# Optimization experiments

Hardware: AMD Instinct MI355X
Metric: run time of the kernel (lower is better)

The kernel has to match this reference:

```python
import jax, jax.numpy as jnp
import numpy as np
from jax import lax

RSM_K = 35
PFM_K = 31


def _box_sum(x, k):
    # Separable zero-padded box sum, equivalent to conv2d with a uniform kxk
    # kernel and padding=k//2 (odd k -> SAME). x: [B,1,H,W]
    p = k // 2
    pad = ((0, 0), (0, 0), (p, p), (0, 0))
    x = lax.reduce_window(x, 0.0, lax.add, (1, 1, k, 1), (1, 1, 1, 1), pad)
    pad = ((0, 0), (0, 0), (0, 0), (p, p))
    x = lax.reduce_window(x, 0.0, lax.add, (1, 1, 1, k), (1, 1, 1, 1), pad)
    return x


def _dilate(x, k):
    # Separable morphological dilation == max_pool2d(kernel=k, stride=1, pad=k//2).
    # -inf padding matches torch's max_pool2d padding semantics for 0/1 masks.
    p = k // 2
    ninf = -jnp.inf
    pad = ((0, 0), (0, 0), (p, p), (0, 0))
    x = lax.reduce_window(x, ninf, lax.max, (1, 1, k, 1), (1, 1, 1, 1), pad)
    pad = ((0, 0), (0, 0), (0, 0), (p, p))
    x = lax.reduce_window(x, ninf, lax.max, (1, 1, 1, k), (1, 1, 1, 1), pad)
    return x


def setup_inputs() -> dict:
    key = jax.random.key(0)
    # Sparse binary lesion mask, values exactly 0.0 / 1.0, shape [B,1,H,W]
    masks = (jax.random.uniform(key, (32, 1, 768, 768)) < 0.02).astype(jnp.float32)
    return {"masks": masks}


def reference(masks):
    # RSM: probability map = uniform 35x35 box average (conv2d with 1/k^2 kernel)
    rsm = _box_sum(masks, RSM_K) * (1.0 / (RSM_K * RSM_K))  # [B,1,H,W]
    # PFM: 1 = lesion, 0 = surrounding (inside 31x31 dilation), 2 = ignore
    dilated = _dilate(masks, PFM_K)
    pfm = jnp.where(masks > 0.5, 1, jnp.where(dilated > 0.5, 0, 2))
    pfm = pfm.astype(jnp.int32)[:, 0, :, :]  # [B,H,W]
    return rsm, pfm
```

## Files before the change

### kernel.cpp

```cpp
#include <hip/hip_runtime.h>


#define BATCH 32
#define HH 768
#define WW 768
#define NPIX (HH * WW)

constexpr int TYO  = 48;
constexpr int HALO = 17;
constexpr int ROWS = TYO + 2 * HALO;
constexpr int NSEG = 12;
constexpr int SSEG = NSEG + 2;
constexpr int NT   = 768;
constexpr int NG   = 4;
constexpr int RPG  = TYO / NG;
constexpr int CT   = 192;

__global__ __launch_bounds__(NT)
void label_gen_fused(const float* __restrict__ in, float* __restrict__ out) {
    __shared__ unsigned long long sbits[ROWS][SSEG];
    __shared__ unsigned int hm[ROWS][CT];

    const int tid  = threadIdx.x;
    const int lane = tid & 63;
    const int wv   = tid >> 6;
    const int y0   = blockIdx.x * TYO;
    const int b    = blockIdx.y;
    const float* __restrict__ src = in + (size_t)b * NPIX;

    for (int lr = wv; lr < ROWS; lr += NT / 64) {
        const int r = y0 - HALO + lr;
        unsigned long long bb[NSEG];
        if ((unsigned)r < (unsigned)HH) {
            const float* rp = src + (size_t)r * WW;
            #pragma unroll
            for (int j = 0; j < NSEG; ++j)
                bb[j] = __ballot(rp[64 * j + lane] > 0.5f);
        } else {
            #pragma unroll
            for (int j = 0; j < NSEG; ++j) bb[j] = 0ull;
        }
        if (lane == 0) {
            sbits[lr][0] = 0ull;
            #pragma unroll
            for (int j = 0; j < NSEG; ++j) sbits[lr][j + 1] = bb[j];
            sbits[lr][SSEG - 1] = 0ull;
        }
    }
    __syncthreads();

    {
        const int r0 = tid / CT;
        const int ct = tid - r0 * CT;
        const int c0 = 4 * ct;
        const int s  = c0 - HALO;
        const int q  = (s >> 6) + 1;
        const int sh = s & 63;
        const unsigned long long M35 = (1ull << 35) - 1;
        for (int lr = r0; lr < ROWS; lr += NG) {
            const unsigned long long w =
                (sbits[lr][q] >> sh) | (sbits[lr][q + 1] << (64 - sh));
            const int h0 = (int)__popcll(w & M35);
            const int h1 = h0 + (int)((w >> 35) & 1) - (int)(w & 1);
            const int h2 = h1 + (int)((w >> 36) & 1) - (int)((w >> 1) & 1);
            const int h3 = h2 + (int)((w >> 37) & 1) - (int)((w >> 2) & 1);
            unsigned long long sm = w | (w >> 1);
            sm |= sm >> 2; sm |= sm >> 4; sm |= sm >> 8;
            const unsigned int o4 = (unsigned int)(((sm >> 2) | (sm >> 17)) & 0xFull);
            const unsigned int m4 = (unsigned int)((w >> 17) & 0xFull);
            const unsigned int mb =
                (((m4 & 1u) | ((m4 & 2u) << 7) | ((m4 & 4u) << 14) | ((m4 & 8u) << 21)) << 6);
            const unsigned int ob =
                (((o4 & 1u) | ((o4 & 2u) << 7) | ((o4 & 4u) << 14) | ((o4 & 8u) << 21)) << 7);
            hm[lr][ct] = (unsigned)h0 | ((unsigned)h1 << 8) | ((unsigned)h2 << 16)
                       | ((unsigned)h3 << 24) | mb | ob;
        }
    }
    __syncthreads();

    const int g   = tid / CT;
    const int ct  = tid - g * CT;
    const int c0  = 4 * ct;
    const int yb  = y0 + RPG * g;
    const int lr0 = RPG * g;

    const unsigned int M6 = 0x003F003Fu;
    const unsigned int M1 = 0x01010101u;

    unsigned int vA = 0, vB = 0;
    unsigned int c31 = 0;
    unsigned int ring_e[2], ring_l[2];
    #pragma unroll
    for (int k = 0; k < 35; ++k) {
        const unsigned int x = hm[lr0 + k][ct];
        vA += x & M6;
        vB += (x >> 8) & M6;
        if (k >= 2 && k <= 32) c31 += (x >> 7) & M1;
        if (k == 0)  ring_l[0] = x;
        if (k == 1)  ring_l[1] = x;
        if (k == 33) ring_e[0] = x;
        if (k == 34) ring_e[1] = x;
    }

    float* orow = out + (size_t)b * NPIX + (size_t)yb * WW + c0;
    float* prow = orow + (size_t)BATCH * NPIX;

    for (int i = 0; i < RPG; ++i) {
        const int lr = lr0 + HALO + i;
        const unsigned int xc = hm[lr][ct];

        float4 r4, p4;
        r4.x = (float)(vA & 0xFFFFu) * (1.0f / 1225.0f);
        r4.y = (float)(vB & 0xFFFFu) * (1.0f / 1225.0f);
        r4.z = (float)(vA >> 16)     * (1.0f / 1225.0f);
        r4.w = (float)(vB >> 16)     * (1.0f / 1225.0f);
        p4.x = ((xc >> 6) & 1u)  ? 1.0f : ((c31 & 0xFFu)         ? 0.0f : 2.0f);
        p4.y = ((xc >> 14) & 1u) ? 1.0f : (((c31 >> 8) & 0xFFu)  ? 0.0f : 2.0f);
        p4.z = ((xc >> 22) & 1u) ? 1.0f : (((c31 >> 16) & 0xFFu) ? 0.0f : 2.0f);
        p4.w = ((xc >> 30) & 1u) ? 1.0f : ((c31 >> 24)           ? 0.0f : 2.0f);

        *(float4*)orow = r4;
        *(float4*)prow = p4;
        orow += WW; prow += WW;

        if (i < RPG - 1) {
            const unsigned int xe   = hm[lr + 18][ct];
            const unsigned int xl31 = hm[lr0 + 2 + i][ct];
            const unsigned int xe31 = ring_e[i & 1];
            const unsigned int xl   = ring_l[i & 1];
            ring_e[i & 1] = xe;
            ring_l[i & 1] = xl31;
            vA  = (vA + (xe & M6)) - (xl & M6);
            vB  = (vB + ((xe >> 8) & M6)) - ((xl >> 8) & M6);
            c31 = (c31 + ((xe31 >> 7) & M1)) - ((xl31 >> 7) & M1);
        }
    }
}

extern "C" void kernel_launch(void* const* d_in, const int* in_sizes, int n_in,
                              void* d_out, int out_size, void* d_ws, size_t ws_size,
                              hipStream_t stream) {
    const float* masks = (const float*)d_in[0];
    float* out = (float*)d_out;
    dim3 grid(HH / TYO, BATCH);
    label_gen_fused<<<grid, NT, 0, stream>>>(masks, out);
}
```

Before: 211.8 us.

## Split fused kernel into horizontal-map and vertical-slide kernels via workspace

Splits the single fused kernel into two launches. The first computes the packed per-row horizontal box counts and mask/dilation bits once per row and writes them to a global workspace. The second reads that workspace and does the vertical sliding-window sums and output writes. This removes the recomputation of the halo rows (34 extra rows per 48-row tile) and the shared-memory footprint, at the cost of a second launch and a workspace round-trip of NPIX/4 words per image. The original fused kernel is kept as a fallback when the workspace is too small.

```diff
diff --git a/kernel.cpp b/kernel.cpp
--- a/kernel.cpp
+++ b/kernel.cpp
@@ -6,108 +6,99 @@
 #define WW 768
 #define NPIX (HH * WW)
 
-constexpr int TYO  = 48;
-constexpr int HALO = 17;
-constexpr int ROWS = TYO + 2 * HALO;
-constexpr int NSEG = 12;
-constexpr int SSEG = NSEG + 2;
-constexpr int NT   = 768;
-constexpr int NG   = 4;
-constexpr int RPG  = TYO / NG;
-constexpr int CT   = 192;
-
-__global__ __launch_bounds__(NT)
-void label_gen_fused(const float* __restrict__ in, float* __restrict__ out) {
-    __shared__ unsigned long long sbits[ROWS][SSEG];
-    __shared__ unsigned int hm[ROWS][CT];
-
-    const int tid  = threadIdx.x;
-    const int lane = tid & 63;
-    const int wv   = tid >> 6;
-    const int y0   = blockIdx.x * TYO;
+constexpr int K1_RPB = 16;
+
+__global__ __launch_bounds__(256)
+void hmap_kernel(const float* __restrict__ in, unsigned int* __restrict__ hmg) {
+    __shared__ unsigned long long sb[4][14];
+    const int lane = threadIdx.x & 63;
+    const int wv   = threadIdx.x >> 6;
     const int b    = blockIdx.y;
+    const int r0   = blockIdx.x * K1_RPB;
     const float* __restrict__ src = in + (size_t)b * NPIX;
-
-    for (int lr = wv; lr < ROWS; lr += NT / 64) {
-        const int r = y0 - HALO + lr;
-        unsigned long long bb[NSEG];
-        if ((unsigned)r < (unsigned)HH) {
-            const float* rp = src + (size_t)r * WW;
-            #pragma unroll
-            for (int j = 0; j < NSEG; ++j)
-                bb[j] = __ballot(rp[64 * j + lane] > 0.5f);
-        } else {
-            #pragma unroll
-            for (int j = 0; j < NSEG; ++j) bb[j] = 0ull;
-        }
+    unsigned int* __restrict__ dst = hmg + (size_t)b * (NPIX / 4);
+    const unsigned long long M35 = (1ull << 35) - 1;
+    auto bit = [](unsigned long long w, int k) -> unsigned {
+        return (unsigned)((w >> k) & 1ull);
+    };
+
+    for (int r = r0 + wv; r < r0 + K1_RPB; r += 4) {
+        const float* rp = src + (size_t)r * WW;
+        unsigned long long bb[12];
+        #pragma unroll
+        for (int j = 0; j < 12; ++j) bb[j] = __ballot(rp[64 * j + lane] > 0.5f);
         if (lane == 0) {
-            sbits[lr][0] = 0ull;
-            #pragma unroll
-            for (int j = 0; j < NSEG; ++j) sbits[lr][j + 1] = bb[j];
-            sbits[lr][SSEG - 1] = 0ull;
-        }
-    }
-    __syncthreads();
-
-    {
-        const int r0 = tid / CT;
-        const int ct = tid - r0 * CT;
-        const int c0 = 4 * ct;
-        const int s  = c0 - HALO;
-        const int q  = (s >> 6) + 1;
-        const int sh = s & 63;
-        const unsigned long long M35 = (1ull << 35) - 1;
-        for (int lr = r0; lr < ROWS; lr += NG) {
+            sb[wv][0] = 0ull;
+            #pragma unroll
+            for (int j = 0; j < 12; ++j) sb[wv][j + 1] = bb[j];
+            sb[wv][13] = 0ull;
+        }
+        __builtin_amdgcn_wave_barrier();
+        #pragma unroll
+        for (int it = 0; it < 3; ++it) {
+            const int gi = it * 64 + lane;
+            const int s  = 4 * gi - 17;
+            const int q  = (s >> 6) + 1;
+            const int sh = s & 63;
             const unsigned long long w =
-                (sbits[lr][q] >> sh) | (sbits[lr][q + 1] << (64 - sh));
-            const int h0 = (int)__popcll(w & M35);
-            const int h1 = h0 + (int)((w >> 35) & 1) - (int)(w & 1);
-            const int h2 = h1 + (int)((w >> 36) & 1) - (int)((w >> 1) & 1);
-            const int h3 = h2 + (int)((w >> 37) & 1) - (int)((w >> 2) & 1);
+                (sb[wv][q] >> sh) | (sb[wv][q + 1] << (64 - sh));
+            const unsigned h0 = (unsigned)__popcll(w & M35);
+            const unsigned h1 = h0 + bit(w, 35) - bit(w, 0);
+            const unsigned h2 = h1 + bit(w, 36) - bit(w, 1);
+            const unsigned h3 = h2 + bit(w, 37) - bit(w, 2);
             unsigned long long sm = w | (w >> 1);
             sm |= sm >> 2; sm |= sm >> 4; sm |= sm >> 8;
-            const unsigned int o4 = (unsigned int)(((sm >> 2) | (sm >> 17)) & 0xFull);
-            const unsigned int m4 = (unsigned int)((w >> 17) & 0xFull);
-            const unsigned int mb =
-                (((m4 & 1u) | ((m4 & 2u) << 7) | ((m4 & 4u) << 14) | ((m4 & 8u) << 21)) << 6);
-            const unsigned int ob =
-                (((o4 & 1u) | ((o4 & 2u) << 7) | ((o4 & 4u) << 14) | ((o4 & 8u) << 21)) << 7);
-            hm[lr][ct] = (unsigned)h0 | ((unsigned)h1 << 8) | ((unsigned)h2 << 16)
-                       | ((unsigned)h3 << 24) | mb | ob;
-        }
-    }
-    __syncthreads();
-
-    const int g   = tid / CT;
-    const int ct  = tid - g * CT;
-    const int c0  = 4 * ct;
+            const unsigned o4 = (unsigned)(((sm >> 2) | (sm >> 17)) & 0xFull);
+            const unsigned m4 = (unsigned)((w >> 17) & 0xFull);
+            const unsigned x = h0 | (h1 << 8) | (h2 << 16) | (h3 << 24)
+                             | ((m4 & 1u) << 6)  | ((m4 & 2u) << 13)
+                             | ((m4 & 4u) << 20) | ((m4 & 8u) << 27)
+                             | ((o4 & 1u) << 7)  | ((o4 & 2u) << 14)
+                             | ((o4 & 4u) << 21) | ((o4 & 8u) << 28);
+            dst[(size_t)r * 192 + gi] = x;
+        }
+        __builtin_amdgcn_wave_barrier();
+    }
+}
+
+constexpr int TYO = 48;
+constexpr int RPG = 12;
+
+__global__ __launch_bounds__(768)
+void vslide_kernel(const unsigned int* __restrict__ hmg, float* __restrict__ out) {
+    const int tid = threadIdx.x;
+    const int g   = tid / 192;
+    const int ct  = tid - g * 192;
+    const int y0  = blockIdx.x * TYO;
+    const int b   = blockIdx.y;
     const int yb  = y0 + RPG * g;
-    const int lr0 = RPG * g;
-
-    const unsigned int M6 = 0x003F003Fu;
-    const unsigned int M1 = 0x01010101u;
-
-    unsigned int vA = 0, vB = 0;
-    unsigned int c31 = 0;
-    unsigned int ring_e[2], ring_l[2];
+    const unsigned int* __restrict__ hb = hmg + (size_t)b * (NPIX / 4) + ct;
+    auto ld = [&](int r) -> unsigned {
+        return ((unsigned)r < (unsigned)HH) ? hb[(size_t)r * 192] : 0u;
+    };
+    const unsigned M6 = 0x003F003Fu;
+    const unsigned M1 = 0x01010101u;
+
+    unsigned vA = 0, vB = 0, c31 = 0;
+    unsigned ring_a[2], ring_s[2];
     #pragma unroll
     for (int k = 0; k < 35; ++k) {
-        const unsigned int x = hm[lr0 + k][ct];
+        const unsigned x = ld(yb - 17 + k);
         vA += x & M6;
         vB += (x >> 8) & M6;
         if (k >= 2 && k <= 32) c31 += (x >> 7) & M1;
-        if (k == 0)  ring_l[0] = x;
-        if (k == 1)  ring_l[1] = x;
-        if (k == 33) ring_e[0] = x;
-        if (k == 34) ring_e[1] = x;
-    }
-
-    float* orow = out + (size_t)b * NPIX + (size_t)yb * WW + c0;
+        if (k == 0)  ring_s[0] = x;
+        if (k == 1)  ring_s[1] = x;
+        if (k == 33) ring_a[0] = x;
+        if (k == 34) ring_a[1] = x;
+    }
+
+    float* orow = out + (size_t)b * NPIX + (size_t)yb * WW + 4 * ct;
     float* prow = orow + (size_t)BATCH * NPIX;
 
     for (int i = 0; i < RPG; ++i) {
-        const int lr = lr0 + HALO + i;
-        const unsigned int xc = hm[lr][ct];
+        const int y = yb + i;
+        const unsigned xc = hb[(size_t)y * 192];
 
         float4 r4, p4;
         r4.x = (float)(vA & 0xFFFFu) * (1.0f / 1225.0f);
@@ -124,10 +115,124 @@
         orow += WW; prow += WW;
 
         if (i < RPG - 1) {
-            const unsigned int xe   = hm[lr + 18][ct];
-            const unsigned int xl31 = hm[lr0 + 2 + i][ct];
-            const unsigned int xe31 = ring_e[i & 1];
-            const unsigned int xl   = ring_l[i & 1];
+            const unsigned xa = ld(y + 18);
+            const unsigned xs = ld(y - 15);
+            const unsigned a31 = ring_a[i & 1];  ring_a[i & 1] = xa;
+            const unsigned s35 = ring_s[i & 1];  ring_s[i & 1] = xs;
+            vA  = (vA + (xa & M6)) - (s35 & M6);
+            vB  = (vB + ((xa >> 8) & M6)) - ((s35 >> 8) & M6);
+            c31 = (c31 + ((a31 >> 7) & M1)) - ((xs >> 7) & M1);
+        }
+    }
+}
+
+constexpr int F_HALO = 17;
+constexpr int F_ROWS = TYO + 2 * F_HALO;
+constexpr int F_SSEG = 14;
+
+__global__ __launch_bounds__(768)
+void label_gen_fused(const float* __restrict__ in, float* __restrict__ out) {
+    __shared__ unsigned long long sbits[F_ROWS][F_SSEG];
+    __shared__ unsigned int hm[F_ROWS][192];
+
+    const int tid  = threadIdx.x;
+    const int lane = tid & 63;
+    const int wv   = tid >> 6;
+    const int y0   = blockIdx.x * TYO;
+    const int b    = blockIdx.y;
+    const float* __restrict__ src = in + (size_t)b * NPIX;
+
+    for (int lr = wv; lr < F_ROWS; lr += 12) {
+        const int r = y0 - F_HALO + lr;
+        unsigned long long bb[12];
+        if ((unsigned)r < (unsigned)HH) {
+            const float* rp = src + (size_t)r * WW;
+            #pragma unroll
+            for (int j = 0; j < 12; ++j) bb[j] = __ballot(rp[64 * j + lane] > 0.5f);
+        } else {
+            #pragma unroll
+            for (int j = 0; j < 12; ++j) bb[j] = 0ull;
+        }
+        if (lane == 0) {
+            sbits[lr][0] = 0ull;
+            #pragma unroll
+            for (int j = 0; j < 12; ++j) sbits[lr][j + 1] = bb[j];
+            sbits[lr][13] = 0ull;
+        }
+    }
+    __syncthreads();
+
+    {
+        const int r0 = tid / 192;
+        const int ct = tid - r0 * 192;
+        const int s  = 4 * ct - 17;
+        const int q  = (s >> 6) + 1;
+        const int sh = s & 63;
+        const unsigned long long M35 = (1ull << 35) - 1;
+        for (int lr = r0; lr < F_ROWS; lr += 4) {
+            const unsigned long long w =
+                (sbits[lr][q] >> sh) | (sbits[lr][q + 1] << (64 - sh));
+            const unsigned h0 = (unsigned)__popcll(w & M35);
+            const unsigned h1 = h0 + (unsigned)((w >> 35) & 1) - (unsigned)(w & 1);
+            const unsigned h2 = h1 + (unsigned)((w >> 36) & 1) - (unsigned)((w >> 1) & 1);
+            const unsigned h3 = h2 + (unsigned)((w >> 37) & 1) - (unsigned)((w >> 2) & 1);
+            unsigned long long sm = w | (w >> 1);
+            sm |= sm >> 2; sm |= sm >> 4; sm |= sm >> 8;
+            const unsigned o4 = (unsigned)(((sm >> 2) | (sm >> 17)) & 0xFull);
+            const unsigned m4 = (unsigned)((w >> 17) & 0xFull);
+            hm[lr][ct] = h0 | (h1 << 8) | (h2 << 16) | (h3 << 24)
+                       | ((m4 & 1u) << 6)  | ((m4 & 2u) << 13)
+                       | ((m4 & 4u) << 20) | ((m4 & 8u) << 27)
+                       | ((o4 & 1u) << 7)  | ((o4 & 2u) << 14)
+                       | ((o4 & 4u) << 21) | ((o4 & 8u) << 28);
+        }
+    }
+    __syncthreads();
+
+    const int g   = tid / 192;
+    const int ct  = tid - g * 192;
+    const int yb  = y0 + RPG * g;
+    const int lr0 = RPG * g;
+    const unsigned M6 = 0x003F003Fu;
+    const unsigned M1 = 0x01010101u;
+
+    unsigned vA = 0, vB = 0, c31 = 0;
+    unsigned ring_e[2], ring_l[2];
+    #pragma unroll
+    for (int k = 0; k < 35; ++k) {
+        const unsigned x = hm[lr0 + k][ct];
+        vA += x & M6;
+        vB += (x >> 8) & M6;
+        if (k >= 2 && k <= 32) c31 += (x >> 7) & M1;
+        if (k == 0)  ring_l[0] = x;
+        if (k == 1)  ring_l[1] = x;
+        if (k == 33) ring_e[0] = x;
+        if (k == 34) ring_e[1] = x;
+    }
+
+    float* orow = out + (size_t)b * NPIX + (size_t)yb * WW + 4 * ct;
+    float* prow = orow + (size_t)BATCH * NPIX;
+
+    for (int i = 0; i < RPG; ++i) {
+        const int lr = lr0 + F_HALO + i;
+        const unsigned xc = hm[lr][ct];
+        float4 r4, p4;
+        r4.x = (float)(vA & 0xFFFFu) * (1.0f / 1225.0f);
+        r4.y = (float)(vB & 0xFFFFu) * (1.0f / 1225.0f);
+        r4.z = (float)(vA >> 16)     * (1.0f / 1225.0f);
+        r4.w = (float)(vB >> 16)     * (1.0f / 1225.0f);
+        p4.x = ((xc >> 6) & 1u)  ? 1.0f : ((c31 & 0xFFu)         ? 0.0f : 2.0f);
+        p4.y = ((xc >> 14) & 1u) ? 1.0f : (((c31 >> 8) & 0xFFu)  ? 0.0f : 2.0f);
+        p4.z = ((xc >> 22) & 1u) ? 1.0f : (((c31 >> 16) & 0xFFu) ? 0.0f : 2.0f);
+        p4.w = ((xc >> 30) & 1u) ? 1.0f : ((c31 >> 24)           ? 0.0f : 2.0f);
+        *(float4*)orow = r4;
+        *(float4*)prow = p4;
+        orow += WW; prow += WW;
+        if (i < RPG - 1) {
+            const unsigned xe   = hm[lr + 18][ct];
+            const unsigned xl31 = hm[lr0 + 2 + i][ct];
+            const unsigned xe31 = ring_e[i & 1];
+            const unsigned xl   = ring_l[i & 1];
             ring_e[i & 1] = xe;
             ring_l[i & 1] = xl31;
             vA  = (vA + (xe & M6)) - (xl & M6);
@@ -142,6 +247,15 @@
                               hipStream_t stream) {
     const float* masks = (const float*)d_in[0];
     float* out = (float*)d_out;
-    dim3 grid(HH / TYO, BATCH);
-    label_gen_fused<<<grid, NT, 0, stream>>>(masks, out);
-}
+    const size_t need = (size_t)BATCH * NPIX;
+    if (ws_size >= need) {
+        unsigned int* hmg = (unsigned int*)d_ws;
+        dim3 g1(HH / K1_RPB, BATCH);
+        hmap_kernel<<<g1, 256, 0, stream>>>(masks, hmg);
+        dim3 g2(HH / TYO, BATCH);
+        vslide_kernel<<<g2, 768, 0, stream>>>(hmg, out);
+    } else {
+        dim3 grid(HH / TYO, BATCH);
+        label_gen_fused<<<grid, 768, 0, stream>>>(masks, out);
+    }
+}
```

Measured after the change: 218.6 us. +3.2%, slower.
